# Optimization experiments

Hardware: AMD Instinct MI355X
Metric: run time of the kernel (lower is better)

The kernel has to match this reference:

```python
import jax, jax.numpy as jnp
import numpy as np

N_CLASSES = 5
IGNORE_LB = 255
MAX_INDEX = 128          # indexes are drawn in [1, MAX_INDEX]
B, D, H, W = 2, 64, 512, 512
S = N_CLASSES * MAX_INDEX + 1   # static segment capacity: key = max*label + index <= max*n_classes


def setup_inputs() -> dict:
    key = jax.random.key(0)
    k1, k2, k3 = jax.random.split(key, 3)
    feature_out = jax.random.normal(k1, (B, D, H, W), dtype=jnp.float32)
    labels = jax.random.randint(k2, (B, H, W), 0, N_CLASSES).astype(jnp.int64)
    indexes = jax.random.randint(k3, (B, H, W), 1, MAX_INDEX + 1).astype(jnp.int64)
    return {"feature_out": feature_out, "labels": labels, "indexes": indexes}


def _huber(r):
    # torch.where(ret < 1, 0.5*ret**2, ret - 0.5)
    return jnp.where(r < 1.0, 0.5 * r * r, r - 0.5)


def _per_image(feat, label, index):
    # feat: [P, D] float; label, index: [P] int
    m = index.max()                                   # torch: max = index_single.max() (before remap)
    ig = label == IGNORE_LB
    lab = jnp.where(ig, 0, label)
    idx = jnp.where(ig, 0, index)
    keyv = (m * lab + idx).astype(jnp.int32)          # combined sort key; ignore pixels -> key 0

    # Segment mean pooling (replaces sort + nonzero + python cat loop).
    counts = jax.ops.segment_sum(jnp.ones(keyv.shape, jnp.float32), keyv, num_segments=S)
    sums = jax.ops.segment_sum(feat, keyv, num_segments=S)        # [S, D]
    means = sums / jnp.maximum(counts, 1.0)[:, None]

    seg = jnp.arange(S)
    # Original keeps only segments with key != 0 (non-ignore) and size >= 2
    # (the `index_range[i+1]-index_range[i] > 1` style checks).
    valid = (counts >= 2.0) & (seg != 0)
    # class of segment key k: ceil(k/max) - 1  (== label for index in [1, max])
    cls = (jnp.ceil(seg.astype(jnp.float32) / m.astype(jnp.float32)) - 1.0).astype(jnp.int32)
    cmask = ((cls[None, :] == jnp.arange(N_CLASSES)[:, None]) & valid[None, :]).astype(jnp.float32)  # [C, S]

    # Pairwise mean-abs-distance between all segment means: A[i,j] = mean_D |m_i - m_j|
    A = jnp.mean(jnp.abs(means[:, None, :] - means[None, :, :]), axis=-1)  # [S, S]

    pairsum = cmask @ A @ cmask.T                      # [C, C] sum of A over (seg in c1, seg in c2)
    n_c = cmask.sum(-1)                                # segments per class
    npair = n_c[:, None] * n_c[None, :]
    ret = pairsum / jnp.maximum(npair, 1.0)            # torch.mean(|x - y|) per class pair
    h = _huber(ret)

    tri = jnp.triu(jnp.ones((N_CLASSES, N_CLASSES), jnp.float32), k=1)
    pv = tri * (npair > 0.0)                           # unordered pairs of non-empty class groups
    return jnp.sum(h * pv), jnp.sum(pv)


def reference(feature_out, labels, indexes):
    Bn = feature_out.shape[0]
    feat = jnp.transpose(feature_out, (0, 2, 3, 1)).reshape(Bn, -1, feature_out.shape[1])  # [B, P, D]
    lab = labels.reshape(Bn, -1)
    idx = indexes.reshape(Bn, -1)
    s, c = jax.vmap(_per_image)(feat, lab, idx)
    tot_s, tot_c = s.sum(), c.sum()
    mean_h = tot_s / jnp.maximum(tot_c, 1.0)           # torch.mean(torch.stack(losses))
    mean_h = jnp.maximum(mean_h, jnp.float32(1e-12))   # guard log(0)
    Bf = jnp.asarray(Bn, jnp.float32)
    # loss = -mean_h; return -log(-loss/B). If no pairs: loss = -B -> -log(1) = 0.
    out = jnp.where(tot_c > 0.0, -jnp.log(mean_h / Bf), jnp.float32(0.0))
    return out.reshape(1)
```

## Files before the change

kernel.cpp:

```cpp
#include <hip/hip_runtime.h>
#include <math.h>

#define BATCH 2
#define DCH 64
#define PIX (512 * 512)
#define NCLS 5
#define IGNORE_LB 255
#define KSTR 129
#define NSEG 645
#define NBLK 64
#define TI 16

#define OFF_PAIR  0
#define OFF_SUM   256
#define ZERO_BYTES 330496
#define OFF_CNT   330496
#define OFF_BASE  335872
#define OFF_BHIST 341248
#define OFF_KEYS  671488
#define OFF_SKEY  1720064
#define OFF_POS   2768640
#define OFF_FEATS 4865792

__global__ void k_zero(float4* __restrict__ p) {
    const int n4 = ZERO_BYTES / 16;
    for (int i = blockIdx.x * blockDim.x + threadIdx.x; i < n4;
         i += gridDim.x * blockDim.x)
        p[i] = make_float4(0.f, 0.f, 0.f, 0.f);
}

__device__ __forceinline__ unsigned short f2bf(float f) {
    unsigned int u = __float_as_uint(f);
    u += 0x7FFFu + ((u >> 16) & 1u);
    return (unsigned short)(u >> 16);
}

__global__ void k_keys(const int* __restrict__ lab, const int* __restrict__ idx,
                       unsigned short* __restrict__ keys,
                       unsigned int* __restrict__ blockHist) {
    __shared__ unsigned int hist[NSEG];
    const int b = blockIdx.y, blk = blockIdx.x;
    for (int i = threadIdx.x; i < NSEG; i += blockDim.x) hist[i] = 0u;
    __syncthreads();
    const int4* lb = (const int4*)(lab + (size_t)b * PIX);
    const int4* ib = (const int4*)(idx + (size_t)b * PIX);
    unsigned short* kb = keys + (size_t)b * PIX;
    #pragma unroll
    for (int it = 0; it < 4; ++it) {
        const int g = blk * 1024 + it * 256 + threadIdx.x;
        const int4 l4 = lb[g];
        const int4 x4 = ib[g];
        int k[4];
        k[0] = (l4.x == IGNORE_LB) ? 0 : KSTR * l4.x + x4.x;
        k[1] = (l4.y == IGNORE_LB) ? 0 : KSTR * l4.y + x4.y;
        k[2] = (l4.z == IGNORE_LB) ? 0 : KSTR * l4.z + x4.z;
        k[3] = (l4.w == IGNORE_LB) ? 0 : KSTR * l4.w + x4.w;
        ushort4 o;
        o.x = (unsigned short)k[0]; o.y = (unsigned short)k[1];
        o.z = (unsigned short)k[2]; o.w = (unsigned short)k[3];
        *(ushort4*)(kb + 4 * g) = o;
        #pragma unroll
        for (int j = 0; j < 4; ++j) atomicAdd(&hist[k[j]], 1u);
    }
    __syncthreads();
    unsigned int* bh = blockHist + ((size_t)b * NBLK + blk) * NSEG;
    for (int i = threadIdx.x; i < NSEG; i += blockDim.x) bh[i] = hist[i];
}

__global__ void k_scan(unsigned int* __restrict__ blockHist,
                       unsigned int* __restrict__ counts,
                       unsigned int* __restrict__ base) {
    __shared__ unsigned int tot[NSEG];
    const int b = blockIdx.x;
    unsigned int* bh = blockHist + (size_t)b * NBLK * NSEG;
    for (int s = threadIdx.x; s < NSEG; s += blockDim.x) {
        unsigned int run = 0u;
        #pragma unroll 8
        for (int blk = 0; blk < NBLK; ++blk) {
            const unsigned int t = bh[(size_t)blk * NSEG + s];
            bh[(size_t)blk * NSEG + s] = run;
            run += t;
        }
        tot[s] = run;
        counts[b * NSEG + s] = run;
    }
    __syncthreads();
    if (threadIdx.x < 64) {
        const int lane = threadIdx.x;
        unsigned int carry = 0u;
        for (int c = 0; c < (NSEG + 63) / 64; ++c) {
            const int s = c * 64 + lane;
            unsigned int v0 = (s < NSEG) ? tot[s] : 0u;
            unsigned int v = v0;
            #pragma unroll
            for (int o = 1; o < 64; o <<= 1) {
                unsigned int t = __shfl_up(v, o, 64);
                if (lane >= o) v += t;
            }
            if (s < NSEG) base[b * NSEG + s] = carry + (v - v0);
            carry += __shfl(v, 63, 64);
        }
    }
}

__global__ void k_scatter(const unsigned short* __restrict__ keys,
                          const unsigned int* __restrict__ blockHist,
                          const unsigned int* __restrict__ base,
                          unsigned int* __restrict__ posOf,
                          unsigned short* __restrict__ skey) {
    __shared__ unsigned int cur[NSEG];
    const int b = blockIdx.y, blk = blockIdx.x;
    const unsigned int* bh = blockHist + ((size_t)b * NBLK + blk) * NSEG;
    for (int s = threadIdx.x; s < NSEG; s += blockDim.x)
        cur[s] = base[b * NSEG + s] + bh[s];
    __syncthreads();
    const unsigned short* kb = keys + (size_t)b * PIX;
    unsigned int* po = posOf + (size_t)b * PIX;
    unsigned short* sk = skey + (size_t)b * PIX;
    #pragma unroll
    for (int it = 0; it < 4; ++it) {
        const int g = blk * 1024 + it * 256 + threadIdx.x;
        const ushort4 k4 = *(const ushort4*)(kb + 4 * g);
        const unsigned short kk[4] = {k4.x, k4.y, k4.z, k4.w};
        #pragma unroll
        for (int j = 0; j < 4; ++j) {
            const unsigned int pos = atomicAdd(&cur[kk[j]], 1u);
            po[4 * g + j] = pos;
            sk[pos] = kk[j];
        }
    }
}

__global__ __launch_bounds__(256) void k_tpose(const float* __restrict__ feat,
                                               const unsigned int* __restrict__ posOf,
                                               unsigned short* __restrict__ featS) {
    __shared__ unsigned short tile[64][72];
    __shared__ unsigned int posLDS[64];
    const int b = blockIdx.y;
    const int P0 = blockIdx.x * 64;
    const int tid = threadIdx.x;
    if (tid < 64) posLDS[tid] = posOf[(size_t)b * PIX + P0 + tid];
    const float* fb = feat + (size_t)b * DCH * PIX;
    #pragma unroll
    for (int i = 0; i < 4; ++i) {
        const int idx = i * 256 + tid;
        const int ch = idx >> 4, px4 = idx & 15;
        const float4 v = *(const float4*)(fb + (size_t)ch * PIX + P0 + 4 * px4);
        tile[4 * px4 + 0][ch] = f2bf(v.x);
        tile[4 * px4 + 1][ch] = f2bf(v.y);
        tile[4 * px4 + 2][ch] = f2bf(v.z);
        tile[4 * px4 + 3][ch] = f2bf(v.w);
    }
    __syncthreads();
    unsigned short* fS = featS + (size_t)b * PIX * DCH;
    #pragma unroll
    for (int i = 0; i < 4; ++i) {
        const int idx = i * 256 + tid;
        const int px = idx >> 4, c4 = idx & 15;
        const unsigned int* t32 = (const unsigned int*)&tile[px][4 * c4];
        uint2 w; w.x = t32[0]; w.y = t32[1];
        *(uint2*)(fS + ((size_t)posLDS[px]) * DCH + 4 * c4) = w;
    }
}

__global__ __launch_bounds__(256) void k_segsum(const unsigned short* __restrict__ featS,
                                                const unsigned short* __restrict__ skey,
                                                float* __restrict__ sums) {
    const int b = blockIdx.y;
    const int lane = threadIdx.x & 63, wid = threadIdx.x >> 6;
    const int q0 = (blockIdx.x * 4 + wid) * 64;
    const unsigned short* fS = featS + (size_t)b * PIX * DCH;
    const int sk = skey[(size_t)b * PIX + q0 + lane];
    int cur = __shfl(sk, 0, 64);
    float acc = 0.f;
    #pragma unroll 8
    for (int j = 0; j < 64; ++j) {
        const int k = __shfl(sk, j, 64);
        const unsigned int u = fS[(size_t)(q0 + j) * DCH + lane];
        const float f = __uint_as_float(u << 16);
        if (k != cur) {
            unsafeAtomicAdd(&sums[((size_t)b * NSEG + cur) * DCH + lane], acc);
            acc = 0.f;
            cur = k;
        }
        acc += f;
    }
    unsafeAtomicAdd(&sums[((size_t)b * NSEG + cur) * DCH + lane], acc);
}

__global__ void k_pairs(const float* __restrict__ sums,
                        const unsigned int* __restrict__ counts,
                        float* __restrict__ pairsum) {
    __shared__ float rI[TI][DCH + 1], rJ[TI][DCH + 1];
    __shared__ int cI[TI], cJ[TI];
    __shared__ float ps[NCLS * NCLS];
    const int b = blockIdx.z;
    const int i0 = blockIdx.x * TI, j0 = blockIdx.y * TI;
    if (threadIdx.x < NCLS * NCLS) ps[threadIdx.x] = 0.f;
    for (int t = threadIdx.x; t < TI * DCH; t += blockDim.x) {
        const int r = t >> 6, d = t & 63;
        const int si = i0 + r, sj = j0 + r;
        float vi = 0.f, vj = 0.f;
        if (si < NSEG) {
            const float c = fmaxf((float)counts[b * NSEG + si], 1.f);
            vi = sums[((size_t)b * NSEG + si) * DCH + d] / c;
        }
        if (sj < NSEG) {
            const float c = fmaxf((float)counts[b * NSEG + sj], 1.f);
            vj = sums[((size_t)b * NSEG + sj) * DCH + d] / c;
        }
        rI[r][d] = vi;
        rJ[r][d] = vj;
    }
    if (threadIdx.x < TI) {
        int si = i0 + threadIdx.x;
        bool ok = (si > 0 && si < NSEG && counts[b * NSEG + si] >= 2u);
        cI[threadIdx.x] = ok ? (si - 1) / KSTR : -1;
        int sj = j0 + threadIdx.x;
        ok = (sj > 0 && sj < NSEG && counts[b * NSEG + sj] >= 2u);
        cJ[threadIdx.x] = ok ? (sj - 1) / KSTR : -1;
    }
    __syncthreads();
    const int ti = threadIdx.x >> 4, tj = threadIdx.x & 15;
    const int ci = cI[ti], cj = cJ[tj];
    if (ci >= 0 && ci < NCLS && cj >= 0 && cj < NCLS) {
        float s = 0.f;
        #pragma unroll
        for (int d = 0; d < DCH; ++d) s += fabsf(rI[ti][d] - rJ[tj][d]);
        unsafeAtomicAdd(&ps[ci * NCLS + cj], s * (1.f / DCH));
    }
    __syncthreads();
    if (threadIdx.x < NCLS * NCLS && ps[threadIdx.x] != 0.f)
        unsafeAtomicAdd(&pairsum[b * NCLS * NCLS + threadIdx.x], ps[threadIdx.x]);
}

__global__ void k_final(const unsigned int* __restrict__ counts,
                        const float* __restrict__ pairsum,
                        float* __restrict__ out) {
    __shared__ int nc[BATCH][NCLS];
    __shared__ float psl[BATCH * NCLS * NCLS];
    const int tid = threadIdx.x;
    if (tid < BATCH * NCLS) nc[tid / NCLS][tid % NCLS] = 0;
    if (tid < BATCH * NCLS * NCLS) psl[tid] = pairsum[tid];
    __syncthreads();
    for (int t = tid; t < BATCH * NSEG; t += blockDim.x) {
        const int b = t / NSEG, s = t % NSEG;
        if (s > 0 && counts[t] >= 2u) {
            const int c = (s - 1) / KSTR;
            if (c >= 0 && c < NCLS) atomicAdd(&nc[b][c], 1);
        }
    }
    __syncthreads();
    if (tid == 0) {
        float tot_s = 0.f, tot_c = 0.f;
        for (int b = 0; b < BATCH; ++b)
            for (int c1 = 0; c1 < NCLS; ++c1)
                for (int c2 = c1 + 1; c2 < NCLS; ++c2) {
                    const float np = (float)nc[b][c1] * (float)nc[b][c2];
                    if (np > 0.f) {
                        const float r = psl[b * NCLS * NCLS + c1 * NCLS + c2] / np;
                        tot_s += (r < 1.f) ? 0.5f * r * r : r - 0.5f;
                        tot_c += 1.f;
                    }
                }
        float mh = tot_s / fmaxf(tot_c, 1.f);
        mh = fmaxf(mh, 1e-12f);
        out[0] = (tot_c > 0.f) ? -logf(mh / (float)BATCH) : 0.f;
    }
}

extern "C" void kernel_launch(void* const* d_in, const int* in_sizes, int n_in,
                              void* d_out, int out_size, void* d_ws, size_t ws_size,
                              hipStream_t stream) {
    const float* feat = (const float*)d_in[0];
    const int* lab = (const int*)d_in[1];
    const int* idx = (const int*)d_in[2];
    float* out = (float*)d_out;
    char* ws = (char*)d_ws;

    float* pairsum        = (float*)(ws + OFF_PAIR);
    float* sums           = (float*)(ws + OFF_SUM);
    unsigned int* counts  = (unsigned int*)(ws + OFF_CNT);
    unsigned int* base    = (unsigned int*)(ws + OFF_BASE);
    unsigned int* bhist   = (unsigned int*)(ws + OFF_BHIST);
    unsigned short* keys  = (unsigned short*)(ws + OFF_KEYS);
    unsigned short* skey  = (unsigned short*)(ws + OFF_SKEY);
    unsigned int* posOf   = (unsigned int*)(ws + OFF_POS);
    unsigned short* featS = (unsigned short*)(ws + OFF_FEATS);

    k_zero<<<81, 256, 0, stream>>>((float4*)ws);
    k_keys<<<dim3(NBLK, BATCH), 256, 0, stream>>>(lab, idx, keys, bhist);
    k_scan<<<BATCH, 256, 0, stream>>>(bhist, counts, base);
    k_scatter<<<dim3(NBLK, BATCH), 256, 0, stream>>>(keys, bhist, base, posOf, skey);
    k_tpose<<<dim3(PIX / 64, BATCH), 256, 0, stream>>>(feat, posOf, featS);
    k_segsum<<<dim3(PIX / 256, BATCH), 256, 0, stream>>>(featS, skey, sums);
    k_pairs<<<dim3((NSEG + TI - 1) / TI, (NSEG + TI - 1) / TI, BATCH), 256, 0, stream>>>(
        sums, counts, pairsum);
    k_final<<<1, 256, 0, stream>>>(counts, pairsum, out);
}
```

Before: 114.9 us.

## Swizzle transpose tile, use nontemporal loads/stores, widen segsum loads, double histogram blocks

The pixel range is split into twice as many histogram/scatter blocks, and the scratch buffer offsets are moved to make room for the larger block histogram. The transpose kernel XOR-swizzles its LDS tile to avoid bank conflicts and uses nontemporal global loads and stores for the streamed feature data. The segment-sum kernel now has each half-wave process alternate pixels with 32-bit (two-bf16) loads, which halves loop iterations but doubles the number of atomics at each segment boundary. More blocks also means a larger block histogram and a larger prefix-scan workload.

```diff
diff --git a/kernel.cpp b/kernel.cpp
--- a/kernel.cpp
+++ b/kernel.cpp
@@ -8,8 +8,11 @@
 #define IGNORE_LB 255
 #define KSTR 129
 #define NSEG 645
-#define NBLK 64
+#define NBLK 128
 #define TI 16
+
+typedef float  vfloat4 __attribute__((ext_vector_type(4)));
+typedef unsigned int vuint2 __attribute__((ext_vector_type(2)));
 
 #define OFF_PAIR  0
 #define OFF_SUM   256
@@ -17,10 +20,10 @@
 #define OFF_CNT   330496
 #define OFF_BASE  335872
 #define OFF_BHIST 341248
-#define OFF_KEYS  671488
-#define OFF_SKEY  1720064
-#define OFF_POS   2768640
-#define OFF_FEATS 4865792
+#define OFF_KEYS  1001728
+#define OFF_SKEY  2050304
+#define OFF_POS   3098880
+#define OFF_FEATS 5196032
 
 __global__ void k_zero(float4* __restrict__ p) {
     const int n4 = ZERO_BYTES / 16;
@@ -46,8 +49,8 @@
     const int4* ib = (const int4*)(idx + (size_t)b * PIX);
     unsigned short* kb = keys + (size_t)b * PIX;
     #pragma unroll
-    for (int it = 0; it < 4; ++it) {
-        const int g = blk * 1024 + it * 256 + threadIdx.x;
+    for (int it = 0; it < 2; ++it) {
+        const int g = blk * 512 + it * 256 + threadIdx.x;
         const int4 l4 = lb[g];
         const int4 x4 = ib[g];
         int k[4];
@@ -118,8 +121,8 @@
     unsigned int* po = posOf + (size_t)b * PIX;
     unsigned short* sk = skey + (size_t)b * PIX;
     #pragma unroll
-    for (int it = 0; it < 4; ++it) {
-        const int g = blk * 1024 + it * 256 + threadIdx.x;
+    for (int it = 0; it < 2; ++it) {
+        const int g = blk * 512 + it * 256 + threadIdx.x;
         const ushort4 k4 = *(const ushort4*)(kb + 4 * g);
         const unsigned short kk[4] = {k4.x, k4.y, k4.z, k4.w};
         #pragma unroll
@@ -145,11 +148,13 @@
     for (int i = 0; i < 4; ++i) {
         const int idx = i * 256 + tid;
         const int ch = idx >> 4, px4 = idx & 15;
-        const float4 v = *(const float4*)(fb + (size_t)ch * PIX + P0 + 4 * px4);
-        tile[4 * px4 + 0][ch] = f2bf(v.x);
-        tile[4 * px4 + 1][ch] = f2bf(v.y);
-        tile[4 * px4 + 2][ch] = f2bf(v.z);
-        tile[4 * px4 + 3][ch] = f2bf(v.w);
+        const vfloat4 v = __builtin_nontemporal_load(
+            (const vfloat4*)(fb + (size_t)ch * PIX + P0 + 4 * px4));
+        const int col = ch ^ ((px4 & 7) << 3);
+        tile[4 * px4 + 0][col] = f2bf(v.x);
+        tile[4 * px4 + 1][col] = f2bf(v.y);
+        tile[4 * px4 + 2][col] = f2bf(v.z);
+        tile[4 * px4 + 3][col] = f2bf(v.w);
     }
     __syncthreads();
     unsigned short* fS = featS + (size_t)b * PIX * DCH;
@@ -157,9 +162,10 @@
     for (int i = 0; i < 4; ++i) {
         const int idx = i * 256 + tid;
         const int px = idx >> 4, c4 = idx & 15;
-        const unsigned int* t32 = (const unsigned int*)&tile[px][4 * c4];
-        uint2 w; w.x = t32[0]; w.y = t32[1];
-        *(uint2*)(fS + ((size_t)posLDS[px]) * DCH + 4 * c4) = w;
+        const int col0 = (4 * c4) ^ (((px >> 2) & 7) << 3);
+        const vuint2 w = *(const vuint2*)&tile[px][col0];
+        __builtin_nontemporal_store(
+            w, (vuint2*)(fS + ((size_t)posLDS[px]) * DCH + 4 * c4));
     }
 }
 
@@ -168,24 +174,30 @@
                                                 float* __restrict__ sums) {
     const int b = blockIdx.y;
     const int lane = threadIdx.x & 63, wid = threadIdx.x >> 6;
+    const int half = lane >> 5, ll = lane & 31;
     const int q0 = (blockIdx.x * 4 + wid) * 64;
     const unsigned short* fS = featS + (size_t)b * PIX * DCH;
     const int sk = skey[(size_t)b * PIX + q0 + lane];
-    int cur = __shfl(sk, 0, 64);
-    float acc = 0.f;
+    int cur = __shfl(sk, half, 64);
+    float acx = 0.f, acy = 0.f;
     #pragma unroll 8
-    for (int j = 0; j < 64; ++j) {
-        const int k = __shfl(sk, j, 64);
-        const unsigned int u = fS[(size_t)(q0 + j) * DCH + lane];
-        const float f = __uint_as_float(u << 16);
+    for (int j = 0; j < 64; j += 2) {
+        const int k = __shfl(sk, j + half, 64);
+        const unsigned int u = __builtin_nontemporal_load(
+            (const unsigned int*)(fS + (size_t)(q0 + j + half) * DCH + 2 * ll));
         if (k != cur) {
-            unsafeAtomicAdd(&sums[((size_t)b * NSEG + cur) * DCH + lane], acc);
-            acc = 0.f;
+            float* dst = &sums[((size_t)b * NSEG + cur) * DCH + 2 * ll];
+            unsafeAtomicAdd(dst, acx);
+            unsafeAtomicAdd(dst + 1, acy);
+            acx = 0.f; acy = 0.f;
             cur = k;
         }
-        acc += f;
-    }
-    unsafeAtomicAdd(&sums[((size_t)b * NSEG + cur) * DCH + lane], acc);
+        acx += __uint_as_float(u << 16);
+        acy += __uint_as_float(u & 0xffff0000u);
+    }
+    float* dst = &sums[((size_t)b * NSEG + cur) * DCH + 2 * ll];
+    unsafeAtomicAdd(dst, acx);
+    unsafeAtomicAdd(dst + 1, acy);
 }
 
 __global__ void k_pairs(const float* __restrict__ sums,
```

Result: slower. 136.3 us (+18.6%).
